# Optimization experiments

Measured on AMD Instinct MI355X. Metric: run time of the kernel, lower is better.

Reference implementation:

```python
import jax, jax.numpy as jnp
import numpy as np

S, B, D, H, WIN, L = 8192, 4, 512, 8, 64, 6
HD = D // H
EPS = 1e-5


def setup_inputs() -> dict:
    key = jax.random.key(0)
    ks = jax.random.split(key, 6)
    s = 0.02
    return {
        "src": jax.random.normal(ks[0], (S, B, D), jnp.float32),
        "Wqkv": jax.random.normal(ks[1], (L, 3 * D, D), jnp.float32) * s,
        "bqkv": jnp.zeros((L, 3 * D), jnp.float32),
        "Wo": jax.random.normal(ks[2], (L, D, D), jnp.float32) * s,
        "bo": jnp.zeros((L, D), jnp.float32),
        "W1": jax.random.normal(ks[3], (L, 4 * D, D), jnp.float32) * s,
        "bf1": jnp.zeros((L, 4 * D), jnp.float32),
        "W2": jax.random.normal(ks[4], (L, D, 4 * D), jnp.float32) * s,
        "bf2": jnp.zeros((L, D), jnp.float32),
        "g1": jnp.ones((L, D), jnp.float32),
        "beta1": jnp.zeros((L, D), jnp.float32),
        "g2": jnp.ones((L, D), jnp.float32),
        "beta2": jnp.zeros((L, D), jnp.float32),
    }


def layernorm(x, g, b):
    m = jnp.mean(x, axis=-1, keepdims=True)
    v = jnp.mean(jnp.square(x - m), axis=-1, keepdims=True)
    return (x - m) * jax.lax.rsqrt(v + EPS) * g + b


def _forward(src, Wqkv, bqkv, Wo, bo, W1, bf1, W2, bf2, g1, beta1, g2, beta2):
    NW = S // WIN
    scale = 1.0 / np.sqrt(HD)
    x = src
    for l in range(L):
        qkv = x @ Wqkv[l].T + bqkv[l]                      # (S,B,3D)
        q, k, v = jnp.split(qkv, 3, axis=-1)
        win = lambda t: t.reshape(NW, WIN, B, H, HD)       # (NW,W,B,H,hd)
        q = win(q) * scale
        k = win(k)
        v = win(v)
        att = jax.nn.softmax(jnp.einsum('nqbhd,nkbhd->nbhqk', q, k), axis=-1)
        o = jnp.einsum('nbhqk,nkbhd->nqbhd', att, v).reshape(S, B, D)
        o = o @ Wo[l].T + bo[l]
        x = layernorm(x + o, g1[l], beta1[l])
        # FFN with ReLU (hidden = 4*d_model)
        f = jax.nn.relu(x @ W1[l].T + bf1[l]) @ W2[l].T + bf2[l]
        x = layernorm(x + f, g2[l], beta2[l])
    return x


def reference(src, Wqkv, bqkv, Wo, bo, W1, bf1, W2, bf2, g1, beta1, g2, beta2):
    return _forward(src, Wqkv, bqkv, Wo, bo, W1, bf1, W2, bf2, g1, beta1, g2, beta2)
```

## Files before the change

kernel.cpp:

```cpp
#include <hip/hip_runtime.h>
#include <hip/hip_bf16.h>

typedef __bf16 bf16x8 __attribute__((ext_vector_type(8)));
typedef float f32x4 __attribute__((ext_vector_type(4)));

static constexpr int NT = 32768;
static constexpr int D_ = 512;
static constexpr int D3 = 1536;
static constexpr int DF = 2048;
static constexpr int L_ = 6;

#define AS1 __attribute__((address_space(1)))
#define AS3 __attribute__((address_space(3)))

__device__ __forceinline__ void gload_lds16(const void* g, void* l) {
  __builtin_amdgcn_global_load_lds((const AS1 void*)g, (AS3 void*)l, 16, 0, 0);
}

template<int K, int NTN, bool RELU>
__global__ __launch_bounds__(256, 3) void gemm128g(
    const __hip_bfloat16* __restrict__ A,
    const __hip_bfloat16* __restrict__ Wp,
    const float* __restrict__ bias,
    __hip_bfloat16* __restrict__ Cout) {
  __shared__ __align__(16) char lds[32768];
  const int t = threadIdx.x;
  const int l = t & 63, w = t >> 6;
  const int lrow = l & 15, lhi = l >> 4;
  const int wr = w >> 1, wc = w & 1;

  const int lin = blockIdx.x;
  const int wg = (lin & 7) * ((int)gridDim.x >> 3) + (lin >> 3);
  const int tm0 = (wg / NTN) * 128, tn0 = (wg % NTN) * 128;

  constexpr int NKT = K / 64;
  constexpr int N = NTN * 128;

  const int srow = t >> 3;
  const int sun = t & 7;
  const int u8 = (sun ^ (srow & 7)) << 3;
  const __hip_bfloat16* sA = A + (size_t)(tm0 + srow) * K + u8;
  const __hip_bfloat16* sA2 = sA + (size_t)64 * K;

  const char* bpB = (const char*)(Wp + (size_t)((tn0 >> 6) + wc) * NKT * 4096) +
                    l * 16;

  const int lo = lrow * 128;
  const int x0 = (lhi ^ (lrow & 7)) << 4;
  const int x1 = ((4 + lhi) ^ (lrow & 7)) << 4;
  const char* pA[2][2];
  pA[0][0] = lds + wr * 8192 + lo + x0;
  pA[0][1] = lds + wr * 8192 + lo + x1;
  pA[1][0] = lds + 16384 + wr * 8192 + lo + x0;
  pA[1][1] = lds + 16384 + wr * 8192 + lo + x1;

  auto stageA = [&](int p, int kt) {
    char* d0 = lds + p * 16384 + w * 1024;
    const __hip_bfloat16* s0 = sA + kt * 64;
    gload_lds16(s0, d0);
    gload_lds16(s0 + (size_t)32 * K, d0 + 4096);
    char* d1 = lds + p * 16384 + 8192 + w * 1024;
    const __hip_bfloat16* s1 = sA2 + kt * 64;
    gload_lds16(s1, d1);
    gload_lds16(s1 + (size_t)32 * K, d1 + 4096);
  };
  auto loadB = [&](bf16x8 (&bf)[4][2], int kt) {
    const char* q = bpB + (size_t)kt * 8192;
#pragma unroll
    for (int n = 0; n < 4; ++n)
#pragma unroll
      for (int ks = 0; ks < 2; ++ks)
        bf[n][ks] = *(const bf16x8*)(q + (n * 2 + ks) * 1024);
  };

  f32x4 acc[4][4] = {};
  bf16x8 bfA[4][2], bfB[4][2], af[2][2];

  stageA(0, 0);
  __builtin_amdgcn_sched_barrier(0);
  loadB(bfA, 0);
  asm volatile("s_waitcnt vmcnt(8)" ::: "memory");
  __builtin_amdgcn_sched_barrier(0);
  __builtin_amdgcn_s_barrier();

#define SUB(P, BF, MB)                                                      \
  {                                                                          \
    _Pragma("unroll") for (int ks = 0; ks < 2; ++ks) {                       \
      af[0][ks] = *(const bf16x8*)(pA[P][ks] + (MB) * 2048);                 \
      af[1][ks] = *(const bf16x8*)(pA[P][ks] + (MB + 1) * 2048);             \
    }                                                                        \
    _Pragma("unroll") for (int n = 0; n < 4; ++n)                            \
        _Pragma("unroll") for (int ks = 0; ks < 2; ++ks) {                   \
      acc[MB][n] = __builtin_amdgcn_mfma_f32_16x16x32_bf16(                  \
          af[0][ks], BF[n][ks], acc[MB][n], 0, 0, 0);                        \
      acc[MB + 1][n] = __builtin_amdgcn_mfma_f32_16x16x32_bf16(              \
          af[1][ks], BF[n][ks], acc[MB + 1][n], 0, 0, 0);                    \
    }                                                                        \
  }
#define CLOSE(VM)                                                           \
  if (VM) asm volatile("s_waitcnt vmcnt(8)" ::: "memory");                  \
  asm volatile("s_waitcnt lgkmcnt(0)" ::: "memory");                        \
  __builtin_amdgcn_sched_barrier(0);                                        \
  __builtin_amdgcn_s_barrier();

  for (int it = 0; it < NKT / 2; ++it) {
    const int k1 = 2 * it + 1;
    const bool more = (it + 1 < NKT / 2);
    stageA(1, k1);
    __builtin_amdgcn_sched_barrier(0);
    loadB(bfB, k1);
    SUB(0, bfA, 0)
    SUB(0, bfA, 2)
    CLOSE(1)
    if (more) {
      stageA(0, k1 + 1);
      __builtin_amdgcn_sched_barrier(0);
      loadB(bfA, k1 + 1);
    }
    SUB(1, bfB, 0)
    SUB(1, bfB, 2)
    CLOSE(more)
  }
#undef SUB
#undef CLOSE

  char* ep = lds + w * 8192;
#pragma unroll
  for (int n = 0; n < 4; ++n) {
    float bv = bias[tn0 + wc * 64 + n * 16 + lrow];
#pragma unroll
    for (int m = 0; m < 4; ++m)
#pragma unroll
      for (int j = 0; j < 4; ++j) {
        float v = acc[m][n][j] + bv;
        if (RELU) v = fmaxf(v, 0.f);
        int row = m * 16 + lhi * 4 + j;
        int col = n * 16 + lrow;
        *(__hip_bfloat16*)(ep + row * 128 + (((col >> 3) ^ (row & 7)) << 4) +
                           (col & 7) * 2) = __float2bfloat16(v);
      }
  }
  __builtin_amdgcn_sched_barrier(0);
  const int er = l >> 3, ec = l & 7;
#pragma unroll
  for (int p = 0; p < 8; ++p) {
    int r = p * 8 + er;
    uint4 vv = *(const uint4*)(ep + r * 128 + ((ec ^ (r & 7)) << 4));
    *(uint4*)&Cout[(size_t)(tm0 + wr * 64 + r) * N + tn0 + wc * 64 + ec * 8] = vv;
  }
}

__global__ __launch_bounds__(128) void attn_win(
    const __hip_bfloat16* __restrict__ qkv, __hip_bfloat16* __restrict__ o) {
  __shared__ __align__(16) char lds[2 * 18432];
  const int t = threadIdx.x, l = t & 63, w = t >> 6;
  char* vt = lds + w * 18432;
  char* pl = vt + 9216;
  const int wid = blockIdx.x * 2 + w;
  const int h = wid & 7, b = (wid >> 3) & 3, nw = wid >> 5;
  const int lrow = l & 15, lhi = l >> 4;
  const __hip_bfloat16* qp = qkv + (size_t)(nw * 256 + b) * 1536 + h * 64;
  const __hip_bfloat16* kp = qp + 512;
  const __hip_bfloat16* vp = qp + 1024;

  {
    const int d0 = (l & 7) * 8;
    const int r0 = l >> 3;
#pragma unroll
    for (int i = 0; i < 8; ++i) {
      int r = r0 + i * 8;
      union { uint4 u; __hip_bfloat16 e[8]; } vv;
      vv.u = *(const uint4*)(vp + (size_t)r * 6144 + d0);
#pragma unroll
      for (int j = 0; j < 8; ++j)
        *(__hip_bfloat16*)(vt + ((d0 + j) * 72 + r) * 2) = vv.e[j];
    }
  }

  bf16x8 qf[4][2], kf[4][2];
#pragma unroll
  for (int mi = 0; mi < 4; ++mi)
#pragma unroll
    for (int ks = 0; ks < 2; ++ks) {
      int r = mi * 16 + lrow;
      int d = ks * 32 + lhi * 8;
      qf[mi][ks] = __builtin_bit_cast(bf16x8, *(const uint4*)(qp + (size_t)r * 6144 + d));
      kf[mi][ks] = __builtin_bit_cast(bf16x8, *(const uint4*)(kp + (size_t)r * 6144 + d));
    }

  f32x4 s[4][4] = {};
#pragma unroll
  for (int mi = 0; mi < 4; ++mi)
#pragma unroll
    for (int ni = 0; ni < 4; ++ni) {
      s[mi][ni] = __builtin_amdgcn_mfma_f32_16x16x32_bf16(qf[mi][0], kf[ni][0], s[mi][ni], 0, 0, 0);
      s[mi][ni] = __builtin_amdgcn_mfma_f32_16x16x32_bf16(qf[mi][1], kf[ni][1], s[mi][ni], 0, 0, 0);
    }

#pragma unroll
  for (int mi = 0; mi < 4; ++mi)
#pragma unroll
    for (int j = 0; j < 4; ++j) {
      float mx = s[mi][0][j];
#pragma unroll
      for (int ni = 1; ni < 4; ++ni) mx = fmaxf(mx, s[mi][ni][j]);
      mx = fmaxf(mx, __shfl_xor(mx, 1));
      mx = fmaxf(mx, __shfl_xor(mx, 2));
      mx = fmaxf(mx, __shfl_xor(mx, 4));
      mx = fmaxf(mx, __shfl_xor(mx, 8));
      float p[4], sum = 0.f;
#pragma unroll
      for (int ni = 0; ni < 4; ++ni) { p[ni] = __expf(s[mi][ni][j] - mx); sum += p[ni]; }
      sum += __shfl_xor(sum, 1);
      sum += __shfl_xor(sum, 2);
      sum += __shfl_xor(sum, 4);
      sum += __shfl_xor(sum, 8);
      float inv = 1.f / sum;
      int row = mi * 16 + lhi * 4 + j;
#pragma unroll
      for (int ni = 0; ni < 4; ++ni)
        *(__hip_bfloat16*)(pl + (row * 72 + ni * 16 + lrow) * 2) =
            __float2bfloat16(p[ni] * inv);
    }

  bf16x8 pf[4][2], vf[4][2];
#pragma unroll
  for (int mi = 0; mi < 4; ++mi)
#pragma unroll
    for (int ks = 0; ks < 2; ++ks)
      pf[mi][ks] = *(const bf16x8*)(pl + ((mi * 16 + lrow) * 72 + ks * 32 + lhi * 8) * 2);
#pragma unroll
  for (int ni = 0; ni < 4; ++ni)
#pragma unroll
    for (int ks = 0; ks < 2; ++ks)
      vf[ni][ks] = *(const bf16x8*)(vt + ((ni * 16 + lrow) * 72 + ks * 32 + lhi * 8) * 2);

  f32x4 acc[4][4] = {};
#pragma unroll
  for (int mi = 0; mi < 4; ++mi)
#pragma unroll
    for (int ni = 0; ni < 4; ++ni) {
      acc[mi][ni] = __builtin_amdgcn_mfma_f32_16x16x32_bf16(pf[mi][0], vf[ni][0], acc[mi][ni], 0, 0, 0);
      acc[mi][ni] = __builtin_amdgcn_mfma_f32_16x16x32_bf16(pf[mi][1], vf[ni][1], acc[mi][ni], 0, 0, 0);
    }

  __hip_bfloat16* op = o + (size_t)(nw * 256 + b) * 512 + h * 64;
#pragma unroll
  for (int mi = 0; mi < 4; ++mi)
#pragma unroll
    for (int ni = 0; ni < 4; ++ni) {
      int col = ni * 16 + lrow;
#pragma unroll
      for (int j = 0; j < 4; ++j) {
        int row = mi * 16 + lhi * 4 + j;
        op[(size_t)row * 2048 + col] = __float2bfloat16(acc[mi][ni][j]);
      }
    }
}

template<bool LAST>
__global__ __launch_bounds__(256) void ln_res_b(
    __hip_bfloat16* __restrict__ xb, const __hip_bfloat16* __restrict__ f,
    const float* __restrict__ g, const float* __restrict__ be,
    float* __restrict__ xout) {
  const int w = threadIdx.x >> 6, l = threadIdx.x & 63;
  const size_t row = (size_t)blockIdx.x * 4 + w;
  const int c = l * 8;
  union { uint4 u; __hip_bfloat16 e[8]; } xa, fa;
  xa.u = *(const uint4*)(xb + row * 512 + c);
  fa.u = *(const uint4*)(f + row * 512 + c);
  float v[8];
#pragma unroll
  for (int j = 0; j < 8; ++j)
    v[j] = __bfloat162float(xa.e[j]) + __bfloat162float(fa.e[j]);
  float sum = 0.f, sq = 0.f;
#pragma unroll
  for (int j = 0; j < 8; ++j) { sum += v[j]; sq += v[j] * v[j]; }
#pragma unroll
  for (int m = 1; m < 64; m <<= 1) {
    sum += __shfl_xor(sum, m);
    sq += __shfl_xor(sq, m);
  }
  float mean = sum * (1.f / 512.f);
  float var = sq * (1.f / 512.f) - mean * mean;
  float rs = rsqrtf(var + 1e-5f);
  float4 g0 = *(const float4*)(g + c);
  float4 g1v = *(const float4*)(g + c + 4);
  float4 e0 = *(const float4*)(be + c);
  float4 e1 = *(const float4*)(be + c + 4);
  float gg[8] = {g0.x, g0.y, g0.z, g0.w, g1v.x, g1v.y, g1v.z, g1v.w};
  float ee[8] = {e0.x, e0.y, e0.z, e0.w, e1.x, e1.y, e1.z, e1.w};
  float y[8];
  union { uint4 u; __hip_bfloat16 e[8]; } hb;
#pragma unroll
  for (int j = 0; j < 8; ++j) {
    y[j] = (v[j] - mean) * rs * gg[j] + ee[j];
    hb.e[j] = __float2bfloat16(y[j]);
  }
  *(uint4*)(xb + row * 512 + c) = hb.u;
  if (LAST) {
    float4 o0 = {y[0], y[1], y[2], y[3]};
    float4 o1 = {y[4], y[5], y[6], y[7]};
    *(float4*)(xout + row * 512 + c) = o0;
    *(float4*)(xout + row * 512 + c + 4) = o1;
  }
}

__global__ void convw(const float* __restrict__ s, __hip_bfloat16* __restrict__ o) {
  int i = blockIdx.x * 256 + threadIdx.x;
  float4 v = ((const float4*)s)[i];
  __hip_bfloat16 hb[4] = {__float2bfloat16(v.x), __float2bfloat16(v.y),
                          __float2bfloat16(v.z), __float2bfloat16(v.w)};
  ((uint2*)o)[i] = *(uint2*)hb;
}

template<int K, int Nw, bool SCALEQ>
__global__ void convs(const float* __restrict__ s, __hip_bfloat16* __restrict__ o) {
  int i = blockIdx.x * 256 + threadIdx.x;
  int e = i * 4;
  int layer = e / (Nw * K);
  int rem = e - layer * (Nw * K);
  int r = rem / K, c = rem - r * K;
  float4 v = ((const float4*)s)[i];
  float sc = (SCALEQ && r < 512) ? 0.125f : 1.f;
  int didx = layer * (Nw * K) + ((r >> 6) * (K >> 6) + (c >> 6)) * 4096 +
             (((r >> 4) & 3) * 2 + ((c >> 5) & 1)) * 512 + ((c >> 3) & 3) * 128 +
             (r & 15) * 8 + (c & 7);
  __hip_bfloat16 hb[4] = {__float2bfloat16(v.x * sc), __float2bfloat16(v.y * sc),
                          __float2bfloat16(v.z * sc), __float2bfloat16(v.w * sc)};
  *(uint2*)(o + didx) = *(uint2*)hb;
}

__global__ void scaleb(const float* __restrict__ b, float* __restrict__ o) {
  int i = blockIdx.x * 256 + threadIdx.x;
  o[i] = b[i] * (((i % 1536) < 512) ? 0.125f : 1.f);
}

extern "C" void kernel_launch(void* const* d_in, const int* in_sizes, int n_in,
                              void* d_out, int out_size, void* d_ws, size_t ws_size,
                              hipStream_t stream) {
  const float* src  = (const float*)d_in[0];
  const float* Wqkv = (const float*)d_in[1];
  const float* bqkv = (const float*)d_in[2];
  const float* Wo   = (const float*)d_in[3];
  const float* bo   = (const float*)d_in[4];
  const float* W1   = (const float*)d_in[5];
  const float* bf1  = (const float*)d_in[6];
  const float* W2   = (const float*)d_in[7];
  const float* bf2  = (const float*)d_in[8];
  const float* g1   = (const float*)d_in[9];
  const float* be1  = (const float*)d_in[10];
  const float* g2   = (const float*)d_in[11];
  const float* be2  = (const float*)d_in[12];
  float* xout = (float*)d_out;

  char* ws = (char*)d_ws;
  size_t off = 0;
  auto alloc = [&](size_t bytes) {
    char* p = ws + off;
    off += (bytes + 255) & ~(size_t)255;
    return p;
  };

  const size_t wq_b = (size_t)L_ * D3 * D_ * 2;
  const size_t wo_b = (size_t)L_ * D_ * D_ * 2;
  const size_t w1_b = (size_t)L_ * DF * D_ * 2;
  const size_t w2_b = (size_t)L_ * D_ * DF * 2;
  const size_t xb_b = (size_t)NT * 512 * 2;
  auto al = [](size_t v) { return (v + 255) & ~(size_t)255; };
  const size_t persist =
      al(wq_b) + al(wo_b) + al(w1_b) + al(w2_b) + al(L_ * D3 * 4) + al(xb_b);

  int CT = NT;
  while (CT > 2048 && persist + (size_t)CT * 5120 + 65536 > ws_size) CT >>= 1;

  __hip_bfloat16* wqkvb = (__hip_bfloat16*)alloc(wq_b);
  __hip_bfloat16* wob   = (__hip_bfloat16*)alloc(wo_b);
  __hip_bfloat16* w1b   = (__hip_bfloat16*)alloc(w1_b);
  __hip_bfloat16* w2b   = (__hip_bfloat16*)alloc(w2_b);
  float*          bqs   = (float*)alloc((size_t)L_ * D3 * 4);
  __hip_bfloat16* xb    = (__hip_bfloat16*)alloc(xb_b);
  __hip_bfloat16* R     = (__hip_bfloat16*)alloc((size_t)CT * 2048 * 2);
  __hip_bfloat16* OB    = (__hip_bfloat16*)alloc((size_t)CT * 512 * 2);

  convw<<<NT * 512 / 4 / 256, 256, 0, stream>>>(src, xb);
  convs<512, 1536, true><<<L_ * D3 * D_ / 4 / 256, 256, 0, stream>>>(Wqkv, wqkvb);
  convs<512, 512, false><<<L_ * D_ * D_ / 4 / 256, 256, 0, stream>>>(Wo, wob);
  convs<512, 2048, false><<<L_ * DF * D_ / 4 / 256, 256, 0, stream>>>(W1, w1b);
  convs<2048, 512, false><<<L_ * D_ * DF / 4 / 256, 256, 0, stream>>>(W2, w2b);
  scaleb<<<L_ * D3 / 256, 256, 0, stream>>>(bqkv, bqs);

  const int nch = NT / CT;
  for (int c = 0; c < nch; ++c) {
    __hip_bfloat16* xm = xb + (size_t)c * CT * 512;
    float* xo = xout + (size_t)c * CT * 512;
    for (int l = 0; l < L_; ++l) {
      gemm128g<512, 12, false><<<(CT / 128) * 12, 256, 0, stream>>>(
          xm, wqkvb + (size_t)l * D3 * D_, bqs + l * D3, R);
      attn_win<<<CT / 16, 128, 0, stream>>>(R, OB);
      gemm128g<512, 4, false><<<(CT / 128) * 4, 256, 0, stream>>>(
          OB, wob + (size_t)l * D_ * D_, bo + l * D_, R);
      ln_res_b<false><<<CT / 4, 256, 0, stream>>>(xm, R, g1 + l * D_,
                                                  be1 + l * D_, xo);
      gemm128g<512, 16, true><<<(CT / 128) * 16, 256, 0, stream>>>(
          xm, w1b + (size_t)l * DF * D_, bf1 + l * DF, R);
      gemm128g<2048, 4, false><<<(CT / 128) * 4, 256, 0, stream>>>(
          R, w2b + (size_t)l * D_ * DF, bf2 + l * D_, OB);
      if (l == L_ - 1)
        ln_res_b<true><<<CT / 4, 256, 0, stream>>>(xm, OB, g2 + l * D_,
                                                   be2 + l * D_, xo);
      else
        ln_res_b<false><<<CT / 4, 256, 0, stream>>>(xm, OB, g2 + l * D_,
                                                    be2 + l * D_, xo);
    }
  }
}
```

Baseline: 1.816 ms.

## Load GEMM A operand directly from global memory, dropping LDS staging pipeline

Replaces the double-buffered LDS staging of the A tile (global_load_lds with swizzle and explicit barriers/waitcnts) with direct per-lane global vector loads of A fragments into registers, in a simple unrolled k-loop. It removes LDS traffic and workgroup barriers, but each A fragment is now read from global/L2 by both column waves, and the hand-tuned software pipelining is lost, leaving the compiler to schedule loads.

Result: slower. 3.196 ms (+76.1%).

```diff
diff --git a/kernel.cpp b/kernel.cpp
--- a/kernel.cpp
+++ b/kernel.cpp
@@ -10,15 +10,8 @@
 static constexpr int DF = 2048;
 static constexpr int L_ = 6;
 
-#define AS1 __attribute__((address_space(1)))
-#define AS3 __attribute__((address_space(3)))
-
-__device__ __forceinline__ void gload_lds16(const void* g, void* l) {
-  __builtin_amdgcn_global_load_lds((const AS1 void*)g, (AS3 void*)l, 16, 0, 0);
-}
-
 template<int K, int NTN, bool RELU>
-__global__ __launch_bounds__(256, 3) void gemm128g(
+__global__ __launch_bounds__(256, 3) void gemm_ag(
     const __hip_bfloat16* __restrict__ A,
     const __hip_bfloat16* __restrict__ Wp,
     const float* __restrict__ bias,
@@ -36,93 +29,37 @@
   constexpr int NKT = K / 64;
   constexpr int N = NTN * 128;
 
-  const int srow = t >> 3;
-  const int sun = t & 7;
-  const int u8 = (sun ^ (srow & 7)) << 3;
-  const __hip_bfloat16* sA = A + (size_t)(tm0 + srow) * K + u8;
-  const __hip_bfloat16* sA2 = sA + (size_t)64 * K;
-
+  const char* pAg =
+      (const char*)A + ((size_t)(tm0 + wr * 64 + lrow) * K + lhi * 8) * 2;
   const char* bpB = (const char*)(Wp + (size_t)((tn0 >> 6) + wc) * NKT * 4096) +
                     l * 16;
 
-  const int lo = lrow * 128;
-  const int x0 = (lhi ^ (lrow & 7)) << 4;
-  const int x1 = ((4 + lhi) ^ (lrow & 7)) << 4;
-  const char* pA[2][2];
-  pA[0][0] = lds + wr * 8192 + lo + x0;
-  pA[0][1] = lds + wr * 8192 + lo + x1;
-  pA[1][0] = lds + 16384 + wr * 8192 + lo + x0;
-  pA[1][1] = lds + 16384 + wr * 8192 + lo + x1;
-
-  auto stageA = [&](int p, int kt) {
-    char* d0 = lds + p * 16384 + w * 1024;
-    const __hip_bfloat16* s0 = sA + kt * 64;
-    gload_lds16(s0, d0);
-    gload_lds16(s0 + (size_t)32 * K, d0 + 4096);
-    char* d1 = lds + p * 16384 + 8192 + w * 1024;
-    const __hip_bfloat16* s1 = sA2 + kt * 64;
-    gload_lds16(s1, d1);
-    gload_lds16(s1 + (size_t)32 * K, d1 + 4096);
-  };
-  auto loadB = [&](bf16x8 (&bf)[4][2], int kt) {
-    const char* q = bpB + (size_t)kt * 8192;
+  f32x4 acc[4][4] = {};
+
+#pragma unroll 2
+  for (int kt = 0; kt < NKT; ++kt) {
+    bf16x8 af[4][2], bf[4][2];
+    const char* qa = pAg + kt * 128;
+#pragma unroll
+    for (int m = 0; m < 4; ++m)
+#pragma unroll
+      for (int ks = 0; ks < 2; ++ks)
+        af[m][ks] = *(const bf16x8*)(qa + (size_t)m * 32 * K + ks * 64);
+    const char* qb = bpB + (size_t)kt * 8192;
 #pragma unroll
     for (int n = 0; n < 4; ++n)
 #pragma unroll
       for (int ks = 0; ks < 2; ++ks)
-        bf[n][ks] = *(const bf16x8*)(q + (n * 2 + ks) * 1024);
-  };
-
-  f32x4 acc[4][4] = {};
-  bf16x8 bfA[4][2], bfB[4][2], af[2][2];
-
-  stageA(0, 0);
-  __builtin_amdgcn_sched_barrier(0);
-  loadB(bfA, 0);
-  asm volatile("s_waitcnt vmcnt(8)" ::: "memory");
-  __builtin_amdgcn_sched_barrier(0);
-  __builtin_amdgcn_s_barrier();
-
-#define SUB(P, BF, MB)                                                      \
-  {                                                                          \
-    _Pragma("unroll") for (int ks = 0; ks < 2; ++ks) {                       \
-      af[0][ks] = *(const bf16x8*)(pA[P][ks] + (MB) * 2048);                 \
-      af[1][ks] = *(const bf16x8*)(pA[P][ks] + (MB + 1) * 2048);             \
-    }                                                                        \
-    _Pragma("unroll") for (int n = 0; n < 4; ++n)                            \
-        _Pragma("unroll") for (int ks = 0; ks < 2; ++ks) {                   \
-      acc[MB][n] = __builtin_amdgcn_mfma_f32_16x16x32_bf16(                  \
-          af[0][ks], BF[n][ks], acc[MB][n], 0, 0, 0);                        \
-      acc[MB + 1][n] = __builtin_amdgcn_mfma_f32_16x16x32_bf16(              \
-          af[1][ks], BF[n][ks], acc[MB + 1][n], 0, 0, 0);                    \
-    }                                                                        \
-  }
-#define CLOSE(VM)                                                           \
-  if (VM) asm volatile("s_waitcnt vmcnt(8)" ::: "memory");                  \
-  asm volatile("s_waitcnt lgkmcnt(0)" ::: "memory");                        \
-  __builtin_amdgcn_sched_barrier(0);                                        \
-  __builtin_amdgcn_s_barrier();
-
-  for (int it = 0; it < NKT / 2; ++it) {
-    const int k1 = 2 * it + 1;
-    const bool more = (it + 1 < NKT / 2);
-    stageA(1, k1);
-    __builtin_amdgcn_sched_barrier(0);
-    loadB(bfB, k1);
-    SUB(0, bfA, 0)
-    SUB(0, bfA, 2)
-    CLOSE(1)
-    if (more) {
-      stageA(0, k1 + 1);
-      __builtin_amdgcn_sched_barrier(0);
-      loadB(bfA, k1 + 1);
-    }
-    SUB(1, bfB, 0)
-    SUB(1, bfB, 2)
-    CLOSE(more)
-  }
-#undef SUB
-#undef CLOSE
+        bf[n][ks] = *(const bf16x8*)(qb + (n * 2 + ks) * 1024);
+#pragma unroll
+    for (int m = 0; m < 4; ++m)
+#pragma unroll
+      for (int n = 0; n < 4; ++n)
+#pragma unroll
+        for (int ks = 0; ks < 2; ++ks)
+          acc[m][n] = __builtin_amdgcn_mfma_f32_16x16x32_bf16(
+              af[m][ks], bf[n][ks], acc[m][n], 0, 0, 0);
+  }
 
   char* ep = lds + w * 8192;
 #pragma unroll
@@ -395,16 +332,16 @@
     __hip_bfloat16* xm = xb + (size_t)c * CT * 512;
     float* xo = xout + (size_t)c * CT * 512;
     for (int l = 0; l < L_; ++l) {
-      gemm128g<512, 12, false><<<(CT / 128) * 12, 256, 0, stream>>>(
+      gemm_ag<512, 12, false><<<(CT / 128) * 12, 256, 0, stream>>>(
           xm, wqkvb + (size_t)l * D3 * D_, bqs + l * D3, R);
       attn_win<<<CT / 16, 128, 0, stream>>>(R, OB);
-      gemm128g<512, 4, false><<<(CT / 128) * 4, 256, 0, stream>>>(
+      gemm_ag<512, 4, false><<<(CT / 128) * 4, 256, 0, stream>>>(
           OB, wob + (size_t)l * D_ * D_, bo + l * D_, R);
       ln_res_b<false><<<CT / 4, 256, 0, stream>>>(xm, R, g1 + l * D_,
                                                   be1 + l * D_, xo);
-      gemm128g<512, 16, true><<<(CT / 128) * 16, 256, 0, stream>>>(
+      gemm_ag<512, 16, true><<<(CT / 128) * 16, 256, 0, stream>>>(
           xm, w1b + (size_t)l * DF * D_, bf1 + l * DF, R);
-      gemm128g<2048, 4, false><<<(CT / 128) * 4, 256, 0, stream>>>(
+      gemm_ag<2048, 4, false><<<(CT / 128) * 4, 256, 0, stream>>>(
           R, w2b + (size_t)l * D_ * DF, bf2 + l * D_, OB);
       if (l == L_ - 1)
         ln_res_b<true><<<CT / 4, 256, 0, stream>>>(xm, OB, g2 + l * D_,
```
